# Kernel optimization log

Hardware: AMD Instinct MI355X
Metric: run time of the kernel (lower is better)

The kernel has to match this reference:

```python
import jax, jax.numpy as jnp
import numpy as np

B, S, H, NH = 4, 2048, 512, 8  # batch, seq, hidden, heads
D = H // NH                    # head dim = 64


def setup_inputs() -> dict:
    key = jax.random.key(0)
    ks = jax.random.split(key, 12)
    wscale = 1.0 / np.sqrt(H)
    mk = lambda k, sh: jax.random.normal(k, sh, jnp.float32)
    return {
        "q": mk(ks[0], (B, S, H)),
        "k": mk(ks[1], (B, S, H)),
        "v": mk(ks[2], (B, S, H)),
        "k_b": mk(ks[3], (B, S, H)),
        "mask": jax.random.randint(ks[4], (B, S), 0, 2).astype(jnp.int32),
        "Wq": mk(ks[5], (H, H)) * wscale, "bq": jnp.zeros((H,), jnp.float32),
        "Wk": mk(ks[6], (H, H)) * wscale, "bk": jnp.zeros((H,), jnp.float32),
        "Wv": mk(ks[7], (H, H)) * wscale, "bv": jnp.zeros((H,), jnp.float32),
        "Wkb": mk(ks[8], (H, H)) * wscale, "bkb": jnp.zeros((H,), jnp.float32),
        "Wo": mk(ks[9], (H, H)) * wscale, "bo": jnp.zeros((H,), jnp.float32),
    }


def _attn(q, k, v, k_b, mask, Wq, bq, Wk, bk, Wv, bv, Wkb, bkb, Wo, bo):
    b, s, h = q.shape
    proj = lambda x, W, bias: (x @ W + bias).reshape(b, s, NH, D).transpose(0, 2, 1, 3)
    qh = proj(q, Wq, bq)      # [b, nh, s, d]
    kh = proj(k, Wk, bk)
    vh = proj(v, Wv, bv)
    kbh = proj(k_b, Wkb, bkb)
    # q@k^T + q@k_b^T == q@(k+k_b)^T, scaled by sqrt(d)
    corr = jnp.einsum('bhqd,bhkd->bhqk', qh, kh + kbh) / jnp.sqrt(jnp.float32(D))
    # torch mask repeat pattern depends only on key index -> broadcast over q and heads
    corr = jnp.where(mask[:, None, None, :] == 0, jnp.float32(-1e9), corr)
    prob = jax.nn.softmax(corr, axis=-1)  # dropout inactive (eval mode)
    hid = jnp.einsum('bhqk,bhkd->bhqd', prob, vh)
    hid = hid.transpose(0, 2, 1, 3).reshape(b, s, h)
    return hid @ Wo + bo


def reference(q, k, v, k_b, mask, Wq, bq, Wk, bk, Wv, bv, Wkb, bkb, Wo, bo):
    return _attn(q, k, v, k_b, mask, Wq, bq, Wk, bk, Wv, bv, Wkb, bkb, Wo, bo)
```

## Files before the change

### kernel.cpp

```cpp
#include <hip/hip_runtime.h>
#include <hip/hip_bf16.h>
#include <math.h>

#define B_  4
#define S_  2048
#define H_  512
#define NH_ 8
#define D_  64

typedef __attribute__((ext_vector_type(8))) short bf16x8;
typedef __attribute__((ext_vector_type(4))) float f32x4;
#define MFMA16(a, b, c) __builtin_amdgcn_mfma_f32_16x16x32_bf16(a, b, c, 0, 0, 0)

__device__ __forceinline__ unsigned short f2bf(float f) {
    union { float f; unsigned int i; } x; x.f = f;
    unsigned int i = x.i;
    i += 0x7fffu + ((i >> 16) & 1u);
    return (unsigned short)(i >> 16);
}
__device__ __forceinline__ unsigned int pk2(float lo, float hi) {
    union { __hip_bfloat162 h; unsigned int u; } c;
    c.h = __float22bfloat162_rn(make_float2(lo, hi));
    return c.u;
}
__device__ __forceinline__ void gl_lds16(const void* g, void* l) {
    __builtin_amdgcn_global_load_lds(
        (const __attribute__((address_space(1))) unsigned int*)g,
        (__attribute__((address_space(3))) unsigned int*)l, 16, 0, 0);
}

__global__ __launch_bounds__(256) void prep_w(
    const float* __restrict__ W0, const float* __restrict__ W1,
    const float* __restrict__ W2, const float* __restrict__ W3,
    unsigned short* __restrict__ Wt)
{
    const float* Ws[4] = {W0, W1, W2, W3};
    const float* W = Ws[blockIdx.z];
    unsigned short* Y = Wt + (size_t)blockIdx.z * H_ * H_;
    __shared__ float Tl[64][68];
    const int t = threadIdx.x;
    const int k0 = blockIdx.y * 64, n0 = blockIdx.x * 64;
    #pragma unroll
    for (int i = 0; i < 4; ++i) {
        const int e = (t + 256 * i) * 4;
        const int r = e >> 6, c = e & 63;
        const float4 a = *(const float4*)(W + (size_t)(k0 + r) * H_ + n0 + c);
        Tl[c + 0][r] = a.x; Tl[c + 1][r] = a.y;
        Tl[c + 2][r] = a.z; Tl[c + 3][r] = a.w;
    }
    __syncthreads();
    #pragma unroll
    for (int i = 0; i < 4; ++i) {
        const int e = (t + 256 * i) * 4;
        const int n = e >> 6, c = e & 63;
        uint2 p;
        p.x = pk2(Tl[n][c + 0], Tl[n][c + 1]);
        p.y = pk2(Tl[n][c + 2], Tl[n][c + 3]);
        *(uint2*)(Y + (size_t)(n0 + n) * H_ + k0 + c) = p;
    }
}

__global__ __launch_bounds__(256, 3) void proj_all(
    const float* __restrict__ q,  const float* __restrict__ k,
    const float* __restrict__ v,  const float* __restrict__ k_b,
    const unsigned short* __restrict__ Wt,
    const float* __restrict__ bq, const float* __restrict__ bk,
    const float* __restrict__ bkb,const float* __restrict__ bv,
    unsigned short* __restrict__ Qf, unsigned short* __restrict__ Kf,
    unsigned short* __restrict__ Vf)
{
    __shared__ __align__(16) unsigned short LB[17408];
    unsigned short* As = LB;
    unsigned short* Bs = LB + 8192;

    const int z = blockIdx.z;
    const float *X, *bias, *X2 = nullptr, *bias2 = nullptr;
    const unsigned short *Wa, *Wb = nullptr;
    unsigned short* Y;
    bool VT = false;
    const size_t WSZ = (size_t)H_ * H_;
    if (z == 0)      { X = q; Wa = Wt;           bias = bq; Y = Qf; }
    else if (z == 1) { X = k; Wa = Wt + WSZ;     bias = bk;
                       X2 = k_b; Wb = Wt + 2 * WSZ; bias2 = bkb; Y = Kf; }
    else             { X = v; Wa = Wt + 3 * WSZ; bias = bv; Y = Vf; VT = true; }

    const int t = threadIdx.x;
    const int w = t >> 6, lane = t & 63;
    const int quad = lane >> 4, l15 = lane & 15;
    const int wr = w >> 1, wc = w & 1;
    const int m0 = blockIdx.x * 128, n0 = blockIdx.y * 128;

    const f32x4 zero = {0.f, 0.f, 0.f, 0.f};
    f32x4 acc[4][4];
    #pragma unroll
    for (int i = 0; i < 4; ++i)
        #pragma unroll
        for (int j = 0; j < 4; ++j) acc[i][j] = zero;

    const int npass = (X2 != nullptr) ? 2 : 1;
    for (int pass = 0; pass < npass; ++pass) {
        const float* Xp = pass ? X2 : X;
        const unsigned short* Wp = pass ? Wb : Wa;
        for (int kb0 = 0; kb0 < H_; kb0 += 64) {
            __syncthreads();
            #pragma unroll
            for (int i = 0; i < 4; ++i) {
                const int c = w * 4 + i;
                const int u = c * 64 + lane;
                const int row = u >> 3;
                const int sc  = ((u & 7) ^ (row & 7)) << 3;
                gl_lds16(Wp + (size_t)(n0 + row) * H_ + kb0 + sc, Bs + c * 512);
            }
            float4 av[8];
            #pragma unroll
            for (int i = 0; i < 8; ++i) {
                const int e = (t + 256 * i) * 4;
                av[i] = *(const float4*)(Xp + (size_t)(m0 + (e >> 6)) * H_ + kb0 + (e & 63));
            }
            #pragma unroll
            for (int i = 0; i < 8; ++i) {
                const int e = (t + 256 * i) * 4;
                const int row = e >> 6, kc = e & 63;
                uint2 p; p.x = pk2(av[i].x, av[i].y); p.y = pk2(av[i].z, av[i].w);
                *(uint2*)&As[row * 64 + ((((kc >> 3) ^ (row & 7)) << 3) | (kc & 7))] = p;
            }
            __syncthreads();
            #pragma unroll
            for (int ks = 0; ks < 2; ++ks) {
                bf16x8 af[4], bfr[4];
                #pragma unroll
                for (int i = 0; i < 4; ++i) {
                    const int row = wr * 64 + i * 16 + l15;
                    af[i] = *(const bf16x8*)&As[row * 64 +
                                (((ks * 4 + quad) ^ (row & 7)) << 3)];
                }
                #pragma unroll
                for (int j = 0; j < 4; ++j) {
                    const int nrw = wc * 64 + j * 16 + l15;
                    bfr[j] = *(const bf16x8*)&Bs[nrw * 64 +
                                (((ks * 4 + quad) ^ (nrw & 7)) << 3)];
                }
                #pragma unroll
                for (int i = 0; i < 4; ++i)
                    #pragma unroll
                    for (int j = 0; j < 4; ++j)
                        acc[i][j] = MFMA16(af[i], bfr[j], acc[i][j]);
            }
        }
    }

    const int bb = m0 >> 11, s0 = m0 & (S_ - 1);
    if (!VT) {
        #pragma unroll
        for (int i = 0; i < 4; ++i)
            #pragma unroll
            for (int r = 0; r < 4; ++r) {
                const int s = s0 + wr * 64 + i * 16 + quad * 4 + r;
                #pragma unroll
                for (int j = 0; j < 4; ++j) {
                    const int nn = n0 + wc * 64 + j * 16 + l15;
                    const int h = nn >> 6, d = nn & 63;
                    float val = acc[i][j][r] + bias[nn];
                    if (bias2) val += bias2[nn];
                    Y[(((size_t)bb * NH_ + h) * S_ + s) * D_ + d] = f2bf(val);
                }
            }
    } else {
        __syncthreads();
        #pragma unroll
        for (int i = 0; i < 4; ++i)
            #pragma unroll
            for (int r = 0; r < 4; ++r) {
                const int ml = wr * 64 + i * 16 + quad * 4 + r;
                #pragma unroll
                for (int j = 0; j < 4; ++j) {
                    const int nl = wc * 64 + j * 16 + l15;
                    LB[nl * 136 + ml] = f2bf(acc[i][j][r] + bias[n0 + nl]);
                }
            }
        __syncthreads();
        const int nr = t >> 1, half = t & 1;
        const int nn = n0 + nr, h = nn >> 6, d = nn & 63;
        const size_t vbase = (((size_t)bb * NH_ + h) * D_ + d) * S_ + s0 + half * 64;
        #pragma unroll
        for (int i = 0; i < 16; ++i)
            *(ushort4*)(Y + vbase + i * 4) =
                *(const ushort4*)&LB[nr * 136 + half * 64 + i * 4];
    }
}

__global__ __launch_bounds__(256) void attn_mfma(
    unsigned short* QHd,
    const unsigned short* __restrict__ Kh, const unsigned short* __restrict__ Vt,
    const int* __restrict__ mask)
{
    const int b = blockIdx.z, h = blockIdx.y;
    const int q0 = blockIdx.x * 128;
    const int t = threadIdx.x;
    const int w = t >> 6, lane = t & 63;
    const int quad = lane >> 4, l15 = lane & 15;

    __shared__ __align__(16) unsigned short KsL[2 * 4096];
    __shared__ __align__(16) unsigned short VsL[2 * 4096];
    __shared__ __align__(16) unsigned short Ps[128 * 64];
    __shared__ float mskf[S_];

    const size_t head = ((size_t)b * NH_ + h) * S_;
    unsigned short* Qbase = QHd + head * D_;
    const unsigned short* Kbase = Kh + head * D_;
    const unsigned short* Vbase = Vt + head * D_;

    for (int i = t; i < S_; i += 256)
        mskf[i] = (mask[b * S_ + i] == 0) ? -1e9f : 0.f;

    bf16x8 qf[2][2];
    #pragma unroll
    for (int rt = 0; rt < 2; ++rt)
        #pragma unroll
        for (int ds = 0; ds < 2; ++ds)
            qf[rt][ds] = *(const bf16x8*)(
                Qbase + (size_t)(q0 + w * 32 + rt * 16 + l15) * D_ + ds * 32 + quad * 8);

    const f32x4 zero = {0.f, 0.f, 0.f, 0.f};
    f32x4 O[2][4];
    #pragma unroll
    for (int rt = 0; rt < 2; ++rt)
        #pragma unroll
        for (int dt = 0; dt < 4; ++dt) O[rt][dt] = zero;
    float lsum[2] = {0.f, 0.f};
    const float SC2 = 0.125f * 1.44269504089f;

    #define STAGE(kt_) do {                                                        \
        const int bf_ = (kt_) & 1, k0_ = (kt_) * 64;                               \
        _Pragma("unroll")                                                          \
        for (int i_ = 0; i_ < 2; ++i_) {                                           \
            const int c_ = w * 2 + i_;                                             \
            const int u_ = c_ * 64 + lane;                                         \
            const int row_ = u_ >> 3;                                              \
            const int sc_ = ((u_ & 7) ^ (row_ & 7)) << 3;                          \
            gl_lds16(Kbase + (size_t)(k0_ + row_) * D_ + sc_,                      \
                     KsL + bf_ * 4096 + c_ * 512);                                 \
            gl_lds16(Vbase + (size_t)row_ * S_ + k0_ + sc_,                        \
                     VsL + bf_ * 4096 + c_ * 512);                                 \
        }                                                                          \
    } while (0)

    STAGE(0);
    __syncthreads();

    for (int kt = 0; kt < S_ / 64; ++kt) {
        const int bf = kt & 1;
        const int k0 = kt * 64;
        if (kt + 1 < S_ / 64) STAGE(kt + 1);

        #pragma unroll
        for (int ct = 0; ct < 4; ++ct) {
            const int krow = ct * 16 + l15;
            const unsigned short* Kb = KsL + bf * 4096 + krow * 64;
            const bf16x8 kf0 = *(const bf16x8*)&Kb[(quad ^ (krow & 7)) << 3];
            const bf16x8 kf1 = *(const bf16x8*)&Kb[((4 + quad) ^ (krow & 7)) << 3];
            const float4 ms4 = *(const float4*)&mskf[k0 + ct * 16 + quad * 4];
            #pragma unroll
            for (int rt = 0; rt < 2; ++rt) {
                f32x4 acc = zero;
                acc = MFMA16(kf0, qf[rt][0], acc);
                acc = MFMA16(kf1, qf[rt][1], acc);
                float pr[4];
                pr[0] = __builtin_amdgcn_exp2f(fmaf(acc[0], SC2, ms4.x));
                pr[1] = __builtin_amdgcn_exp2f(fmaf(acc[1], SC2, ms4.y));
                pr[2] = __builtin_amdgcn_exp2f(fmaf(acc[2], SC2, ms4.z));
                pr[3] = __builtin_amdgcn_exp2f(fmaf(acc[3], SC2, ms4.w));
                lsum[rt] += (pr[0] + pr[1]) + (pr[2] + pr[3]);
                uint2 pw; pw.x = pk2(pr[0], pr[1]); pw.y = pk2(pr[2], pr[3]);
                const int prow = w * 32 + rt * 16 + l15;
                const int unit = (ct * 2 + (quad >> 1)) ^ (prow & 7);
                *(uint2*)&Ps[prow * 64 + unit * 8 + (quad & 1) * 4] = pw;
            }
        }
        bf16x8 pf[2][2];
        #pragma unroll
        for (int rt = 0; rt < 2; ++rt) {
            const int prow = w * 32 + rt * 16 + l15;
            pf[rt][0] = *(const bf16x8*)&Ps[prow * 64 + ((quad ^ (prow & 7)) << 3)];
            pf[rt][1] = *(const bf16x8*)&Ps[prow * 64 + (((4 + quad) ^ (prow & 7)) << 3)];
        }
        #pragma unroll
        for (int dt = 0; dt < 4; ++dt) {
            const int vrow = dt * 16 + l15;
            const unsigned short* Vb = VsL + bf * 4096 + vrow * 64;
            const bf16x8 vf0 = *(const bf16x8*)&Vb[(quad ^ (vrow & 7)) << 3];
            const bf16x8 vf1 = *(const bf16x8*)&Vb[((4 + quad) ^ (vrow & 7)) << 3];
            #pragma unroll
            for (int rt = 0; rt < 2; ++rt) {
                O[rt][dt] = MFMA16(pf[rt][0], vf0, O[rt][dt]);
                O[rt][dt] = MFMA16(pf[rt][1], vf1, O[rt][dt]);
            }
        }
        __syncthreads();
    }
    #undef STAGE

    #pragma unroll
    for (int rt = 0; rt < 2; ++rt) {
        lsum[rt] += __shfl_xor(lsum[rt], 16, 64);
        lsum[rt] += __shfl_xor(lsum[rt], 32, 64);
    }
    float inv[2][4];
    #pragma unroll
    for (int rt = 0; rt < 2; ++rt)
        #pragma unroll
        for (int r = 0; r < 4; ++r)
            inv[rt][r] = 1.f / __shfl(lsum[rt], quad * 4 + r, 64);
    #pragma unroll
    for (int rt = 0; rt < 2; ++rt)
        #pragma unroll
        for (int dt = 0; dt < 4; ++dt)
            #pragma unroll
            for (int r = 0; r < 4; ++r) {
                const int row = w * 32 + rt * 16 + quad * 4 + r;
                Qbase[(size_t)(q0 + row) * D_ + dt * 16 + l15] =
                    f2bf(O[rt][dt][r] * inv[rt][r]);
            }
}

__global__ __launch_bounds__(256) void out_mfma(
    const unsigned short* __restrict__ Hd, const unsigned short* __restrict__ Wot,
    const float* __restrict__ bias, float* __restrict__ Out)
{
    __shared__ __align__(16) unsigned short As[8192];
    __shared__ __align__(16) unsigned short Bs[4096];
    const int t = threadIdx.x;
    const int w = t >> 6, lane = t & 63;
    const int quad = lane >> 4, l15 = lane & 15;
    const int wr = w >> 1, wc = w & 1;
    const int m0 = blockIdx.x * 128, n0 = blockIdx.y * 64;
    const int bb = m0 >> 11, s0 = m0 & (S_ - 1);

    const f32x4 zero = {0.f, 0.f, 0.f, 0.f};
    f32x4 acc[4][2];
    #pragma unroll
    for (int i = 0; i < 4; ++i)
        #pragma unroll
        for (int j = 0; j < 2; ++j) acc[i][j] = zero;

    for (int kb0 = 0; kb0 < H_; kb0 += 64) {
        const int hk = kb0 >> 6;
        const unsigned short* Ab = Hd + (((size_t)bb * NH_ + hk) * S_ + s0) * D_;
        __syncthreads();
        #pragma unroll
        for (int i = 0; i < 4; ++i) {
            const int c = w * 4 + i, u = c * 64 + lane, row = u >> 3;
            const int sc = ((u & 7) ^ (row & 7)) << 3;
            gl_lds16(Ab + (size_t)row * D_ + sc, As + c * 512);
        }
        #pragma unroll
        for (int i = 0; i < 2; ++i) {
            const int c = w * 2 + i, u = c * 64 + lane, row = u >> 3;
            const int sc = ((u & 7) ^ (row & 7)) << 3;
            gl_lds16(Wot + (size_t)(n0 + row) * H_ + kb0 + sc, Bs + c * 512);
        }
        __syncthreads();
        #pragma unroll
        for (int ks = 0; ks < 2; ++ks) {
            bf16x8 af[4], bfr[2];
            #pragma unroll
            for (int i = 0; i < 4; ++i) {
                const int row = wr * 64 + i * 16 + l15;
                af[i] = *(const bf16x8*)&As[row * 64 +
                            (((ks * 4 + quad) ^ (row & 7)) << 3)];
            }
            #pragma unroll
            for (int j = 0; j < 2; ++j) {
                const int nrw = wc * 32 + j * 16 + l15;
                bfr[j] = *(const bf16x8*)&Bs[nrw * 64 +
                            (((ks * 4 + quad) ^ (nrw & 7)) << 3)];
            }
            #pragma unroll
            for (int i = 0; i < 4; ++i)
                #pragma unroll
                for (int j = 0; j < 2; ++j)
                    acc[i][j] = MFMA16(af[i], bfr[j], acc[i][j]);
        }
    }
    #pragma unroll
    for (int i = 0; i < 4; ++i)
        #pragma unroll
        for (int r = 0; r < 4; ++r) {
            const int m = m0 + wr * 64 + i * 16 + quad * 4 + r;
            #pragma unroll
            for (int j = 0; j < 2; ++j) {
                const int n = n0 + wc * 32 + j * 16 + l15;
                Out[(size_t)m * H_ + n] = acc[i][j][r] + bias[n];
            }
        }
}

__global__ void fill_kernel(float* __restrict__ out, float val, int n) {
    const int i = blockIdx.x * 256 + threadIdx.x;
    if (i < n) out[i] = val;
}

extern "C" void kernel_launch(void* const* d_in, const int* in_sizes, int n_in,
                              void* d_out, int out_size, void* d_ws, size_t ws_size,
                              hipStream_t stream) {
    const float* q   = (const float*)d_in[0];
    const float* k   = (const float*)d_in[1];
    const float* v   = (const float*)d_in[2];
    const float* k_b = (const float*)d_in[3];
    const int*   msk = (const int*)d_in[4];
    const float* Wq  = (const float*)d_in[5];
    const float* bq  = (const float*)d_in[6];
    const float* Wk  = (const float*)d_in[7];
    const float* bk  = (const float*)d_in[8];
    const float* Wv  = (const float*)d_in[9];
    const float* bv  = (const float*)d_in[10];
    const float* Wkb = (const float*)d_in[11];
    const float* bkb = (const float*)d_in[12];
    const float* Wo  = (const float*)d_in[13];
    const float* bo  = (const float*)d_in[14];
    float* out = (float*)d_out;

    const size_t PER  = (size_t)B_ * NH_ * S_ * D_;
    const size_t NEED = 3 * PER * sizeof(unsigned short);
    if (ws_size < NEED) {
        fill_kernel<<<(out_size + 255) / 256, 256, 0, stream>>>(
            out, (float)((ws_size >> 20) + 2), out_size);
        return;
    }
    unsigned short* wsh = (unsigned short*)d_ws;
    unsigned short* Qf  = wsh;
    unsigned short* Kf  = wsh + PER;
    unsigned short* Vf  = wsh + 2 * PER;

    unsigned short* Wt = (unsigned short*)d_out;

    dim3 gw(8, 8, 4);
    prep_w<<<gw, 256, 0, stream>>>(Wq, Wk, Wkb, Wv, Wt);

    dim3 gp((B_ * S_) / 128, H_ / 128, 3);
    proj_all<<<gp, 256, 0, stream>>>(q, k, v, k_b, Wt, bq, bk, bkb, bv, Qf, Kf, Vf);

    dim3 ga(S_ / 128, NH_, B_);
    attn_mfma<<<ga, 256, 0, stream>>>(Qf, Kf, Vf, msk);

    dim3 gw1(8, 8, 1);
    prep_w<<<gw1, 256, 0, stream>>>(Wo, Wo, Wo, Wo, Kf);

    dim3 go((B_ * S_) / 128, H_ / 64, 1);
    out_mfma<<<go, 256, 0, stream>>>(Qf, Kf, bo, out);
}
```

Before: 242.2 us.

## Switch attention to 32x32x16 MFMA with register-resident P via permlane32 swap

Rewrites the attention inner loop to use 32x32x16 bf16 MFMA tiles computing S^T so each lane holds one query row. The P fragment is rebuilt in registers with v_permlane32_swap instead of a round trip through shared memory, which removes the Ps LDS buffer and its writes and reads. It also adds s_setprio around the MFMA sections and simplifies the row-sum reduction and output stores into packed bf16 writes. The register layout change is intricate and raises per-thread accumulator pressure.

```diff
diff --git a/kernel.cpp b/kernel.cpp
--- a/kernel.cpp
+++ b/kernel.cpp
@@ -10,7 +10,9 @@
 
 typedef __attribute__((ext_vector_type(8))) short bf16x8;
 typedef __attribute__((ext_vector_type(4))) float f32x4;
+typedef __attribute__((ext_vector_type(16))) float f32x16;
 #define MFMA16(a, b, c) __builtin_amdgcn_mfma_f32_16x16x32_bf16(a, b, c, 0, 0, 0)
+#define MFMA32(a, b, c) __builtin_amdgcn_mfma_f32_32x32x16_bf16(a, b, c, 0, 0, 0)
 
 __device__ __forceinline__ unsigned short f2bf(float f) {
     union { float f; unsigned int i; } x; x.f = f;
@@ -198,11 +200,10 @@
     const int q0 = blockIdx.x * 128;
     const int t = threadIdx.x;
     const int w = t >> 6, lane = t & 63;
-    const int quad = lane >> 4, l15 = lane & 15;
+    const int hi = lane >> 5, l31 = lane & 31;
 
     __shared__ __align__(16) unsigned short KsL[2 * 4096];
     __shared__ __align__(16) unsigned short VsL[2 * 4096];
-    __shared__ __align__(16) unsigned short Ps[128 * 64];
     __shared__ float mskf[S_];
 
     const size_t head = ((size_t)b * NH_ + h) * S_;
@@ -213,21 +214,16 @@
     for (int i = t; i < S_; i += 256)
         mskf[i] = (mask[b * S_ + i] == 0) ? -1e9f : 0.f;
 
-    bf16x8 qf[2][2];
-    #pragma unroll
-    for (int rt = 0; rt < 2; ++rt)
-        #pragma unroll
-        for (int ds = 0; ds < 2; ++ds)
-            qf[rt][ds] = *(const bf16x8*)(
-                Qbase + (size_t)(q0 + w * 32 + rt * 16 + l15) * D_ + ds * 32 + quad * 8);
-
-    const f32x4 zero = {0.f, 0.f, 0.f, 0.f};
-    f32x4 O[2][4];
-    #pragma unroll
-    for (int rt = 0; rt < 2; ++rt)
-        #pragma unroll
-        for (int dt = 0; dt < 4; ++dt) O[rt][dt] = zero;
-    float lsum[2] = {0.f, 0.f};
+    bf16x8 qf[4];
+    #pragma unroll
+    for (int ks = 0; ks < 4; ++ks)
+        qf[ks] = *(const bf16x8*)(
+            Qbase + (size_t)(q0 + w * 32 + l31) * D_ + ks * 16 + hi * 8);
+
+    f32x16 O0, O1;
+    #pragma unroll
+    for (int i = 0; i < 16; ++i) { O0[i] = 0.f; O1[i] = 0.f; }
+    float lsum = 0.f;
     const float SC2 = 0.125f * 1.44269504089f;
 
     #define STAGE(kt_) do {                                                        \
@@ -253,74 +249,84 @@
         const int k0 = kt * 64;
         if (kt + 1 < S_ / 64) STAGE(kt + 1);
 
-        #pragma unroll
-        for (int ct = 0; ct < 4; ++ct) {
-            const int krow = ct * 16 + l15;
+        bf16x8 pfrag[4];
+        #pragma unroll
+        for (int kb = 0; kb < 2; ++kb) {
+            f32x16 acc;
+            #pragma unroll
+            for (int i = 0; i < 16; ++i) acc[i] = 0.f;
+            const int krow = kb * 32 + l31;
             const unsigned short* Kb = KsL + bf * 4096 + krow * 64;
-            const bf16x8 kf0 = *(const bf16x8*)&Kb[(quad ^ (krow & 7)) << 3];
-            const bf16x8 kf1 = *(const bf16x8*)&Kb[((4 + quad) ^ (krow & 7)) << 3];
-            const float4 ms4 = *(const float4*)&mskf[k0 + ct * 16 + quad * 4];
-            #pragma unroll
-            for (int rt = 0; rt < 2; ++rt) {
-                f32x4 acc = zero;
-                acc = MFMA16(kf0, qf[rt][0], acc);
-                acc = MFMA16(kf1, qf[rt][1], acc);
-                float pr[4];
-                pr[0] = __builtin_amdgcn_exp2f(fmaf(acc[0], SC2, ms4.x));
-                pr[1] = __builtin_amdgcn_exp2f(fmaf(acc[1], SC2, ms4.y));
-                pr[2] = __builtin_amdgcn_exp2f(fmaf(acc[2], SC2, ms4.z));
-                pr[3] = __builtin_amdgcn_exp2f(fmaf(acc[3], SC2, ms4.w));
-                lsum[rt] += (pr[0] + pr[1]) + (pr[2] + pr[3]);
-                uint2 pw; pw.x = pk2(pr[0], pr[1]); pw.y = pk2(pr[2], pr[3]);
-                const int prow = w * 32 + rt * 16 + l15;
-                const int unit = (ct * 2 + (quad >> 1)) ^ (prow & 7);
-                *(uint2*)&Ps[prow * 64 + unit * 8 + (quad & 1) * 4] = pw;
-            }
-        }
-        bf16x8 pf[2][2];
-        #pragma unroll
-        for (int rt = 0; rt < 2; ++rt) {
-            const int prow = w * 32 + rt * 16 + l15;
-            pf[rt][0] = *(const bf16x8*)&Ps[prow * 64 + ((quad ^ (prow & 7)) << 3)];
-            pf[rt][1] = *(const bf16x8*)&Ps[prow * 64 + (((4 + quad) ^ (prow & 7)) << 3)];
-        }
-        #pragma unroll
-        for (int dt = 0; dt < 4; ++dt) {
-            const int vrow = dt * 16 + l15;
+            const int rwk = krow & 7;
+            __builtin_amdgcn_s_setprio(1);
+            #pragma unroll
+            for (int ks = 0; ks < 4; ++ks) {
+                const bf16x8 kf = *(const bf16x8*)&Kb[(((ks * 2 + hi) ^ rwk) << 3)];
+                acc = MFMA32(kf, qf[ks], acc);
+            }
+            __builtin_amdgcn_s_setprio(0);
+            float p[16];
+            #pragma unroll
+            for (int bq = 0; bq < 4; ++bq) {
+                const float4 ms4 = *(const float4*)&mskf[k0 + kb * 32 + bq * 8 + hi * 4];
+                p[4 * bq + 0] = __builtin_amdgcn_exp2f(fmaf(acc[4 * bq + 0], SC2, ms4.x));
+                p[4 * bq + 1] = __builtin_amdgcn_exp2f(fmaf(acc[4 * bq + 1], SC2, ms4.y));
+                p[4 * bq + 2] = __builtin_amdgcn_exp2f(fmaf(acc[4 * bq + 2], SC2, ms4.z));
+                p[4 * bq + 3] = __builtin_amdgcn_exp2f(fmaf(acc[4 * bq + 3], SC2, ms4.w));
+            }
+            lsum += ((p[0] + p[1]) + (p[2] + p[3])) + ((p[4] + p[5]) + (p[6] + p[7]))
+                  + ((p[8] + p[9]) + (p[10] + p[11])) + ((p[12] + p[13]) + (p[14] + p[15]));
+            unsigned pkv[8];
+            #pragma unroll
+            for (int bq = 0; bq < 4; ++bq) {
+                pkv[2 * bq + 0] = pk2(p[4 * bq + 0], p[4 * bq + 1]);
+                pkv[2 * bq + 1] = pk2(p[4 * bq + 2], p[4 * bq + 3]);
+            }
+            #pragma unroll
+            for (int ksl = 0; ksl < 2; ++ksl) {
+                unsigned m0 = pkv[4 * ksl + 0], m2 = pkv[4 * ksl + 2];
+                asm volatile("v_permlane32_swap_b32 %0, %1" : "+v"(m0), "+v"(m2));
+                unsigned m1 = pkv[4 * ksl + 1], m3 = pkv[4 * ksl + 3];
+                asm volatile("v_permlane32_swap_b32 %0, %1" : "+v"(m1), "+v"(m3));
+                union { unsigned u[4]; bf16x8 v; } pu;
+                pu.u[0] = m0; pu.u[1] = m1; pu.u[2] = m2; pu.u[3] = m3;
+                pfrag[kb * 2 + ksl] = pu.v;
+            }
+        }
+        __builtin_amdgcn_s_setprio(1);
+        #pragma unroll
+        for (int dblk = 0; dblk < 2; ++dblk) {
+            const int vrow = dblk * 32 + l31;
             const unsigned short* Vb = VsL + bf * 4096 + vrow * 64;
-            const bf16x8 vf0 = *(const bf16x8*)&Vb[(quad ^ (vrow & 7)) << 3];
-            const bf16x8 vf1 = *(const bf16x8*)&Vb[((4 + quad) ^ (vrow & 7)) << 3];
-            #pragma unroll
-            for (int rt = 0; rt < 2; ++rt) {
-                O[rt][dt] = MFMA16(pf[rt][0], vf0, O[rt][dt]);
-                O[rt][dt] = MFMA16(pf[rt][1], vf1, O[rt][dt]);
-            }
-        }
+            const int rwv = vrow & 7;
+            #pragma unroll
+            for (int ks = 0; ks < 4; ++ks) {
+                const bf16x8 vf = *(const bf16x8*)&Vb[(((ks * 2 + hi) ^ rwv) << 3)];
+                if (dblk == 0) O0 = MFMA32(vf, pfrag[ks], O0);
+                else           O1 = MFMA32(vf, pfrag[ks], O1);
+            }
+        }
+        __builtin_amdgcn_s_setprio(0);
         __syncthreads();
     }
     #undef STAGE
 
-    #pragma unroll
-    for (int rt = 0; rt < 2; ++rt) {
-        lsum[rt] += __shfl_xor(lsum[rt], 16, 64);
-        lsum[rt] += __shfl_xor(lsum[rt], 32, 64);
-    }
-    float inv[2][4];
-    #pragma unroll
-    for (int rt = 0; rt < 2; ++rt)
-        #pragma unroll
-        for (int r = 0; r < 4; ++r)
-            inv[rt][r] = 1.f / __shfl(lsum[rt], quad * 4 + r, 64);
-    #pragma unroll
-    for (int rt = 0; rt < 2; ++rt)
-        #pragma unroll
-        for (int dt = 0; dt < 4; ++dt)
-            #pragma unroll
-            for (int r = 0; r < 4; ++r) {
-                const int row = w * 32 + rt * 16 + quad * 4 + r;
-                Qbase[(size_t)(q0 + row) * D_ + dt * 16 + l15] =
-                    f2bf(O[rt][dt][r] * inv[rt][r]);
-            }
+    lsum += __shfl_xor(lsum, 32, 64);
+    const float inv = 1.f / lsum;
+
+    unsigned short* Orow = Qbase + (size_t)(q0 + w * 32 + l31) * D_;
+    #pragma unroll
+    for (int dblk = 0; dblk < 2; ++dblk) {
+        #pragma unroll
+        for (int bq = 0; bq < 4; ++bq) {
+            const float v0 = (dblk ? O1[4 * bq + 0] : O0[4 * bq + 0]) * inv;
+            const float v1 = (dblk ? O1[4 * bq + 1] : O0[4 * bq + 1]) * inv;
+            const float v2 = (dblk ? O1[4 * bq + 2] : O0[4 * bq + 2]) * inv;
+            const float v3 = (dblk ? O1[4 * bq + 3] : O0[4 * bq + 3]) * inv;
+            uint2 st; st.x = pk2(v0, v1); st.y = pk2(v2, v3);
+            *(uint2*)&Orow[dblk * 32 + bq * 8 + hi * 4] = st;
+        }
+    }
 }
 
 __global__ __launch_bounds__(256) void out_mfma(
```

Result: faster. 232.8 us (-3.9%).
